# Optimization experiments

Measured on AMD Instinct MI355X. Metric: run time of the kernel, lower is better.

Reference implementation:

```python
import jax, jax.numpy as jnp
import numpy as np

N, C = 8192, 64

def setup_inputs() -> dict:
    key = jax.random.key(0)
    k1, k2, k3 = jax.random.split(key, 3)
    values = jax.random.normal(k1, (N, C), dtype=jnp.float32)
    coords = jax.random.uniform(k2, (N, 2), dtype=jnp.float32)
    spacing = jax.random.uniform(k3, (2,), dtype=jnp.float32)
    shift = jnp.zeros((2,), dtype=jnp.float32)
    return {"values": values, "coords": coords, "spacing": spacing, "shift": shift}


def reference(values, coords, spacing, shift):
    # grid_mode branch of upsample_nn: 3 shifted copies of the coord grid
    x, y = coords[:, 0], coords[:, 1]
    new_coords = jnp.concatenate([
        jnp.stack((x + spacing[0], y + spacing[1]), axis=1),
        jnp.stack((x, y + spacing[1]), axis=1),
        jnp.stack((x + spacing[0], y), axis=1),
    ], axis=0)  # [3N, 2]

    # Diffs = ||(new_coords - shift)[:,None] - coords[None,:]||, argmin over coords.
    # argmin of the L2 norm == argmin of the squared distance, so use the
    # expanded form to avoid materializing the [3N, N, 2] difference tensor.
    a = new_coords - shift  # [3N, 2]
    d2 = (jnp.sum(a * a, axis=1)[:, None]
          + jnp.sum(coords * coords, axis=1)[None, :]
          - 2.0 * a @ coords.T)  # [3N, N]
    idx = jnp.argmin(d2, axis=1)  # [3N]
    new_values = values[idx]      # [3N, C]

    out_values = jnp.concatenate([values, new_values], axis=0)   # [4N, C]
    out_coords = jnp.concatenate([coords, new_coords], axis=0)   # [4N, 2]
    return out_values, out_coords
```

## Files before the change

### kernel.cpp

```cpp
#include <hip/hip_runtime.h>

#pragma clang fp contract(off)

#define N_PTS 8192
#define C_DIM 64
#define NQ (3 * N_PTS)
#define G 64
#define NCELL (G * G)
#define MARGIN 1.2e-5f
#define HCELL (1.0f / 64.0f)
#define QBLOCKS (NQ / 32)
#define COPYBLKS 128


__device__ __forceinline__ unsigned int fsortkey(float f) {
    const unsigned int u = __float_as_uint(f);
    return (u & 0x80000000u) ? ~u : (u | 0x80000000u);
}
__device__ __forceinline__ float finvkey(unsigned int e) {
    const unsigned int u = (e & 0x80000000u) ? (e & 0x7fffffffu) : ~e;
    return __uint_as_float(u);
}

__device__ __forceinline__ void shift_query(int g, float x, float y,
                                            float sx, float sy,
                                            float& nx, float& ny) {
    if (g == 0)      { nx = x + sx; ny = y + sy; }
    else if (g == 1) { nx = x;      ny = y + sy; }
    else             { nx = x + sx; ny = y; }
}

__global__ __launch_bounds__(1024) void build_copy_kernel(
    const float2* __restrict__ coords2,
    const float4* __restrict__ values4,
    float4* __restrict__ sorted,
    int* __restrict__ starts,
    float4* __restrict__ out_values4,
    float2* __restrict__ out_coords)
{
#pragma clang fp contract(off)
    if (blockIdx.x > 0) {
        const int t   = threadIdx.x;
        const int row = ((int)blockIdx.x - 1) * 64 + (t >> 4);
        const int c4  = t & 15;
        out_values4[row * 16 + c4] = values4[row * 16 + c4];
        if (c4 == 0) out_coords[row] = coords2[row];
        return;
    }

    __shared__ unsigned int lhist[NCELL];
    __shared__ unsigned int wsum[16];
    const int t    = threadIdx.x;
    const int lane = t & 63;
    const int w    = t >> 6;

    #pragma unroll
    for (int k = 0; k < 4; ++k) lhist[4 * t + k] = 0u;
    __syncthreads();

    float2 cpt[8];
    int    cell[8];
    #pragma unroll
    for (int k = 0; k < 8; ++k) {
        const int i = t + 1024 * k;
        const float2 c = coords2[i];
        cpt[k] = c;
        int cx = (int)(c.x * 64.0f); cx = min(max(cx, 0), G - 1);
        int cy = (int)(c.y * 64.0f); cy = min(max(cy, 0), G - 1);
        cell[k] = cy * G + cx;
        atomicAdd(&lhist[cell[k]], 1u);
    }
    __syncthreads();

    const unsigned h0 = lhist[4 * t + 0], h1 = lhist[4 * t + 1];
    const unsigned h2 = lhist[4 * t + 2], h3 = lhist[4 * t + 3];
    const unsigned tot = h0 + h1 + h2 + h3;

    unsigned v = tot;
    #pragma unroll
    for (int s = 1; s < 64; s <<= 1) {
        const unsigned o = __shfl_up(v, s, 64);
        if (lane >= s) v += o;
    }
    if (lane == 63) wsum[w] = v;
    __syncthreads();
    if (t < 16) {
        unsigned x = wsum[t];
        #pragma unroll
        for (int s = 1; s < 16; s <<= 1) {
            const unsigned o = __shfl_up(x, s, 16);
            if ((t & 15) >= s) x += o;
        }
        wsum[t] = x;
    }
    __syncthreads();
    const unsigned woff = (w == 0) ? 0u : wsum[w - 1];
    const unsigned e0 = v + woff - tot;
    const unsigned e1 = e0 + h0, e2 = e1 + h1, e3 = e2 + h2;
    starts[4 * t + 0] = (int)e0; starts[4 * t + 1] = (int)e1;
    starts[4 * t + 2] = (int)e2; starts[4 * t + 3] = (int)e3;
    lhist[4 * t + 0] = e0; lhist[4 * t + 1] = e1;
    lhist[4 * t + 2] = e2; lhist[4 * t + 3] = e3;
    if (t == 0) starts[NCELL] = N_PTS;
    __syncthreads();

    #pragma unroll
    for (int k = 0; k < 8; ++k) {
        const int i = t + 1024 * k;
        const float2 c = cpt[k];
        const unsigned pos = atomicAdd(&lhist[cell[k]], 1u);
        const float p0 = c.x * c.x;
        const float p1 = c.y * c.y;
        const float sc = p0 + p1;
        sorted[pos] = make_float4(c.x, c.y, sc, __int_as_float(i));
    }
}

__global__ __launch_bounds__(256) void query_kernel(
    const float4* __restrict__ sorted,
    const int* __restrict__ starts,
    const float4* __restrict__ values4,
    const float* __restrict__ spacing,
    const float* __restrict__ shift,
    float4* __restrict__ out_values4,
    float2* __restrict__ out_coords)
{
#pragma clang fp contract(off)
    const int lane = threadIdx.x & 7;
    const int q    = blockIdx.x * 32 + (threadIdx.x >> 3);
    const int g    = q >> 13;
    const int k    = q & (N_PTS - 1);

    const float4 me = sorted[k];
    const int b = __float_as_int(me.w);

    float nx, ny;
    shift_query(g, me.x, me.y, spacing[0], spacing[1], nx, ny);
    const float ax = nx - shift[0];
    const float ay = ny - shift[1];
    const float sa = (ax * ax) + (ay * ay);

    int cx = (int)floorf(ax * 64.0f); cx = min(max(cx, 0), G - 1);
    int cy = (int)floorf(ay * 64.0f); cy = min(max(cy, 0), G - 1);
    const float dxo = fmaxf(fmaxf(ax - 1.0f, -ax), 0.0f);

    float best = INFINITY;
    int   bi   = 0x7fffffff;

#define EVAL_SPAN(S, E)                                                     \
    for (int i = (S) + lane; i < (E); i += 8) {                             \
        const float4 pt = sorted[i];                                        \
        const float p   = ax * pt.x;                                        \
        const float dv  = __builtin_fmaf(ay, pt.y, p);                      \
        const float t1  = sa + pt.z;                                        \
        const float d2  = t1 - (2.0f * dv);                                 \
        const int   j   = __float_as_int(pt.w);                             \
        if (d2 < best || (d2 == best && j < bi)) { best = d2; bi = j; }     \
    }

    const int xa = max(cx - 1, 0), xb = min(cx + 1, G - 1);
    const int ya = max(cy - 1, 0), yb = min(cy + 1, G - 1);
    int ss1[3], ee1[3];
    #pragma unroll
    for (int r = 0; r < 3; ++r) {
        const int yy = ya + r;
        const bool vv = (yy <= yb);
        ss1[r] = vv ? starts[yy * G + xa] : 0;
        ee1[r] = vv ? starts[yy * G + xb + 1] : 0;
    }
    #pragma unroll
    for (int r = 0; r < 3; ++r) {
        EVAL_SPAN(ss1[r], ee1[r])
    }

    unsigned long long key =
        ((unsigned long long)fsortkey(best) << 32) | (unsigned int)bi;
    #pragma unroll
    for (int m = 1; m < 8; m <<= 1) {
        const unsigned long long o = __shfl_xor(key, m, 8);
        if (o < key) key = o;
    }
    best = finvkey((unsigned int)(key >> 32));
    bi   = (int)(unsigned int)key;

    const float U = best + MARGIN;

    float sr = sqrtf(fmaxf(U - dxo * dxo, 0.0f));
    sr = fminf(sr, 4.0f);
    const int ylo = max((int)floorf((ay - sr) * 64.0f), 0);
    const int yhi = min((int)floorf((ay + sr) * 64.0f), G - 1);

    float scw = fminf(sqrtf(U), 4.0f);
    const int xlo_c = max((int)floorf((ax - scw) * 64.0f), 0);
    const int xhi_c = min((int)floorf((ax + scw) * 64.0f), G - 1);

    const bool skip = (ylo >= ya) && (yhi <= yb) && (xlo_c >= xa) && (xhi_c <= xb);

    if (!skip) {
        for (int yy0 = ylo; yy0 <= yhi; yy0 += 4) {
            int ss2[4], ee2[4];
            #pragma unroll
            for (int r = 0; r < 4; ++r) {
                const int yy = yy0 + r;
                bool vv = (yy <= yhi);
                const float ry0 = (float)yy * HCELL;
                const float vy  = fmaxf(fmaxf(ay - ry0 - HCELL, ry0 - ay), 0.0f);
                const float r2  = U - vy * vy;
                vv = vv && (r2 >= 0.0f);
                const float s = fminf(sqrtf(fmaxf(r2, 0.0f)), 4.0f);
                int xl = max((int)floorf((ax - s) * 64.0f), 0);
                int xh = min((int)floorf((ax + s) * 64.0f), G - 1);
                vv = vv && (xl <= xh);
                vv = vv && !(yy >= ya && yy <= yb && xl >= xa && xh <= xb);
                ss2[r] = vv ? starts[yy * G + xl] : 0;
                ee2[r] = vv ? starts[yy * G + xh + 1] : 0;
            }
            #pragma unroll
            for (int r = 0; r < 4; ++r) {
                EVAL_SPAN(ss2[r], ee2[r])
            }
        }
        key = ((unsigned long long)fsortkey(best) << 32) | (unsigned int)bi;
        #pragma unroll
        for (int m = 1; m < 8; m <<= 1) {
            const unsigned long long o = __shfl_xor(key, m, 8);
            if (o < key) key = o;
        }
        bi = (int)(unsigned int)key;
    }
#undef EVAL_SPAN

    const int qi  = g * N_PTS + b;
    const int row = N_PTS + qi;
    out_values4[row * 16 + 2 * lane + 0] = values4[bi * 16 + 2 * lane + 0];
    out_values4[row * 16 + 2 * lane + 1] = values4[bi * 16 + 2 * lane + 1];
    if (lane == 0) out_coords[row] = make_float2(nx, ny);
}

extern "C" void kernel_launch(void* const* d_in, const int* in_sizes, int n_in,
                              void* d_out, int out_size, void* d_ws, size_t ws_size,
                              hipStream_t stream)
{
    const float* values  = (const float*)d_in[0];
    const float* coords  = (const float*)d_in[1];
    const float* spacing = (const float*)d_in[2];
    const float* shift   = (const float*)d_in[3];

    float* out_values = (float*)d_out;
    float2* out_coords = (float2*)(out_values + (size_t)4 * N_PTS * C_DIM);

    char* ws = (char*)d_ws;
    float4* sorted = (float4*)ws;
    int* starts    = (int*)(ws + 131072);

    build_copy_kernel<<<1 + COPYBLKS, 1024, 0, stream>>>(
        (const float2*)coords, (const float4*)values,
        sorted, starts, (float4*)out_values, out_coords);

    query_kernel<<<QBLOCKS, 256, 0, stream>>>(
        sorted, starts, (const float4*)values, spacing, shift,
        (float4*)out_values, out_coords);
}
```

Measured before the change: 24.59 us.

## Split grid build across 16 stripe blocks and stage cell starts in LDS

The counting-sort grid build now runs across 16 blocks instead of one. Each block owns a stripe of 256 cells, computes its global base by counting the points that fall in lower cells, and scatters only its own points. This removes the single-block serial build from the critical path, but every block rereads all coordinates. The query kernel also copies the full starts array (4097 ints) into shared memory per block before its neighbour searches, which trades a per-block load and a barrier for cheaper span lookups.

```diff
diff --git a/kernel.cpp b/kernel.cpp
--- a/kernel.cpp
+++ b/kernel.cpp
@@ -10,6 +10,8 @@
 #define MARGIN 1.2e-5f
 #define HCELL (1.0f / 64.0f)
 #define QBLOCKS (NQ / 32)
+#define STRIPEBLKS 16
+#define CPS (NCELL / STRIPEBLKS)
 #define COPYBLKS 128
 
 
@@ -39,27 +41,31 @@
     float2* __restrict__ out_coords)
 {
 #pragma clang fp contract(off)
-    if (blockIdx.x > 0) {
-        const int t   = threadIdx.x;
-        const int row = ((int)blockIdx.x - 1) * 64 + (t >> 4);
+    const int t = threadIdx.x;
+    if (blockIdx.x >= STRIPEBLKS) {
+        const int row = ((int)blockIdx.x - STRIPEBLKS) * 64 + (t >> 4);
         const int c4  = t & 15;
         out_values4[row * 16 + c4] = values4[row * 16 + c4];
         if (c4 == 0) out_coords[row] = coords2[row];
         return;
     }
 
-    __shared__ unsigned int lhist[NCELL];
-    __shared__ unsigned int wsum[16];
-    const int t    = threadIdx.x;
-    const int lane = t & 63;
-    const int w    = t >> 6;
-
-    #pragma unroll
-    for (int k = 0; k < 4; ++k) lhist[4 * t + k] = 0u;
+    __shared__ unsigned int lhist[CPS];
+    __shared__ unsigned int wred[16];
+    __shared__ unsigned int wsum2[4];
+    __shared__ unsigned int baseSh;
+
+    const int b      = blockIdx.x;
+    const int myBase = b * CPS;
+    const int lane   = t & 63;
+    const int w      = t >> 6;
+
+    if (t < CPS) lhist[t] = 0u;
     __syncthreads();
 
     float2 cpt[8];
     int    cell[8];
+    int cnt = 0;
     #pragma unroll
     for (int k = 0; k < 8; ++k) {
         const int i = t + 1024 * k;
@@ -68,51 +74,58 @@
         int cx = (int)(c.x * 64.0f); cx = min(max(cx, 0), G - 1);
         int cy = (int)(c.y * 64.0f); cy = min(max(cy, 0), G - 1);
         cell[k] = cy * G + cx;
-        atomicAdd(&lhist[cell[k]], 1u);
-    }
-    __syncthreads();
-
-    const unsigned h0 = lhist[4 * t + 0], h1 = lhist[4 * t + 1];
-    const unsigned h2 = lhist[4 * t + 2], h3 = lhist[4 * t + 3];
-    const unsigned tot = h0 + h1 + h2 + h3;
-
-    unsigned v = tot;
-    #pragma unroll
-    for (int s = 1; s < 64; s <<= 1) {
-        const unsigned o = __shfl_up(v, s, 64);
-        if (lane >= s) v += o;
-    }
-    if (lane == 63) wsum[w] = v;
-    __syncthreads();
-    if (t < 16) {
-        unsigned x = wsum[t];
+        cnt += (cell[k] < myBase) ? 1 : 0;
+        const int lc = cell[k] - myBase;
+        if (lc >= 0 && lc < CPS) atomicAdd(&lhist[lc], 1u);
+    }
+
+    int cv = cnt;
+    #pragma unroll
+    for (int s = 32; s >= 1; s >>= 1) cv += __shfl_xor(cv, s, 64);
+    if (lane == 0) wred[w] = (unsigned)cv;
+    __syncthreads();
+    if (t == 0) {
+        unsigned s = 0;
         #pragma unroll
-        for (int s = 1; s < 16; s <<= 1) {
-            const unsigned o = __shfl_up(x, s, 16);
-            if ((t & 15) >= s) x += o;
-        }
-        wsum[t] = x;
-    }
-    __syncthreads();
-    const unsigned woff = (w == 0) ? 0u : wsum[w - 1];
-    const unsigned e0 = v + woff - tot;
-    const unsigned e1 = e0 + h0, e2 = e1 + h1, e3 = e2 + h2;
-    starts[4 * t + 0] = (int)e0; starts[4 * t + 1] = (int)e1;
-    starts[4 * t + 2] = (int)e2; starts[4 * t + 3] = (int)e3;
-    lhist[4 * t + 0] = e0; lhist[4 * t + 1] = e1;
-    lhist[4 * t + 2] = e2; lhist[4 * t + 3] = e3;
-    if (t == 0) starts[NCELL] = N_PTS;
+        for (int j = 0; j < 16; ++j) s += wred[j];
+        baseSh = s;
+    }
+    __syncthreads();
+    const unsigned base = baseSh;
+
+    unsigned h = 0, v = 0;
+    if (t < CPS) {
+        h = lhist[t];
+        v = h;
+        #pragma unroll
+        for (int s = 1; s < 64; s <<= 1) {
+            const unsigned o = __shfl_up(v, s, 64);
+            if (lane >= s) v += o;
+        }
+        if (lane == 63) wsum2[w] = v;
+    }
+    __syncthreads();
+    if (t < CPS) {
+        unsigned woff = 0;
+        for (int j = 0; j < w; ++j) woff += wsum2[j];
+        const unsigned excl = base + woff + v - h;
+        starts[myBase + t] = (int)excl;
+        lhist[t] = excl;
+    }
+    if (b == 0 && t == 0) starts[NCELL] = N_PTS;
     __syncthreads();
 
     #pragma unroll
     for (int k = 0; k < 8; ++k) {
-        const int i = t + 1024 * k;
-        const float2 c = cpt[k];
-        const unsigned pos = atomicAdd(&lhist[cell[k]], 1u);
-        const float p0 = c.x * c.x;
-        const float p1 = c.y * c.y;
-        const float sc = p0 + p1;
-        sorted[pos] = make_float4(c.x, c.y, sc, __int_as_float(i));
+        const int lc = cell[k] - myBase;
+        if (lc >= 0 && lc < CPS) {
+            const unsigned pos = atomicAdd(&lhist[lc], 1u);
+            const float p0 = cpt[k].x * cpt[k].x;
+            const float p1 = cpt[k].y * cpt[k].y;
+            const float sc = p0 + p1;
+            const int i = t + 1024 * k;
+            sorted[pos] = make_float4(cpt[k].x, cpt[k].y, sc, __int_as_float(i));
+        }
     }
 }
 
@@ -126,14 +139,19 @@
     float2* __restrict__ out_coords)
 {
 #pragma clang fp contract(off)
-    const int lane = threadIdx.x & 7;
-    const int q    = blockIdx.x * 32 + (threadIdx.x >> 3);
+    __shared__ int s_starts[NCELL + 1];
+
+    const int tid  = threadIdx.x;
+    const int lane = tid & 7;
+    const int q    = blockIdx.x * 32 + (tid >> 3);
     const int g    = q >> 13;
     const int k    = q & (N_PTS - 1);
 
     const float4 me = sorted[k];
+
+    for (int i = tid; i <= NCELL; i += 256) s_starts[i] = starts[i];
+
     const int b = __float_as_int(me.w);
-
     float nx, ny;
     shift_query(g, me.x, me.y, spacing[0], spacing[1], nx, ny);
     const float ax = nx - shift[0];
@@ -143,6 +161,8 @@
     int cx = (int)floorf(ax * 64.0f); cx = min(max(cx, 0), G - 1);
     int cy = (int)floorf(ay * 64.0f); cy = min(max(cy, 0), G - 1);
     const float dxo = fmaxf(fmaxf(ax - 1.0f, -ax), 0.0f);
+
+    __syncthreads();
 
     float best = INFINITY;
     int   bi   = 0x7fffffff;
@@ -165,8 +185,8 @@
     for (int r = 0; r < 3; ++r) {
         const int yy = ya + r;
         const bool vv = (yy <= yb);
-        ss1[r] = vv ? starts[yy * G + xa] : 0;
-        ee1[r] = vv ? starts[yy * G + xb + 1] : 0;
+        ss1[r] = vv ? s_starts[yy * G + xa] : 0;
+        ee1[r] = vv ? s_starts[yy * G + xb + 1] : 0;
     }
     #pragma unroll
     for (int r = 0; r < 3; ++r) {
@@ -212,8 +232,8 @@
                 int xh = min((int)floorf((ax + s) * 64.0f), G - 1);
                 vv = vv && (xl <= xh);
                 vv = vv && !(yy >= ya && yy <= yb && xl >= xa && xh <= xb);
-                ss2[r] = vv ? starts[yy * G + xl] : 0;
-                ee2[r] = vv ? starts[yy * G + xh + 1] : 0;
+                ss2[r] = vv ? s_starts[yy * G + xl] : 0;
+                ee2[r] = vv ? s_starts[yy * G + xh + 1] : 0;
             }
             #pragma unroll
             for (int r = 0; r < 4; ++r) {
@@ -253,7 +273,7 @@
     float4* sorted = (float4*)ws;
     int* starts    = (int*)(ws + 131072);
 
-    build_copy_kernel<<<1 + COPYBLKS, 1024, 0, stream>>>(
+    build_copy_kernel<<<STRIPEBLKS + COPYBLKS, 1024, 0, stream>>>(
         (const float2*)coords, (const float4*)values,
         sorted, starts, (float4*)out_values, out_coords);
 
```

Result: faster. 23.56 us (-4.2%).
